# Performance work log

Hardware: AMD Instinct MI355X
Metric: run time of the kernel (lower is better)

Reference implementation:

```python
import jax, jax.numpy as jnp
import numpy as np

F_IN, D_MODEL, D_STATE, D_CONV, EXPAND = 20, 256, 64, 4, 2
D_INNER = EXPAND * D_MODEL  # 512
DT_RANK = D_MODEL // 16     # 16
BATCH, SEQ = 64, 1024


def setup_inputs() -> dict:
    key = jax.random.key(0)
    ks = jax.random.split(key, 12)
    s = lambda k, shape, sc: jax.random.normal(k, shape, dtype=jnp.float32) * sc
    inp = {
        "x": jax.random.normal(ks[0], (BATCH, SEQ, F_IN), dtype=jnp.float32),
        "embed_w": s(ks[1], (F_IN, D_MODEL), 0.1),
        "embed_b": jnp.zeros((D_MODEL,), jnp.float32),
        "in_proj_w": s(ks[2], (D_MODEL, 2 * D_INNER), 0.05),
        "conv_w": s(ks[3], (D_CONV, D_INNER), 0.2),
        "conv_b": jnp.zeros((D_INNER,), jnp.float32),
        "x_proj_w": s(ks[4], (D_INNER, DT_RANK + 2 * D_STATE), 0.05),
        "dt_proj_w": s(ks[5], (DT_RANK, D_INNER), 0.1),
        "dt_proj_b": jnp.full((D_INNER,), -4.6, jnp.float32),  # softplus ~ 0.01
        "A_log": jnp.log(jnp.tile(jnp.arange(1, D_STATE + 1, dtype=jnp.float32), (D_INNER, 1))),
        "D": jnp.ones((D_INNER,), jnp.float32),
        "out_proj_w": s(ks[6], (D_INNER, D_MODEL), 0.05),
        "ln_g": jnp.ones((D_MODEL,), jnp.float32),
        "ln_b": jnp.zeros((D_MODEL,), jnp.float32),
        "reg1_w": s(ks[7], (D_MODEL, 64), 0.1),
        "reg1_b": jnp.zeros((64,), jnp.float32),
        "reg2_w": s(ks[8], (64, 1), 0.1),
        "reg2_b": jnp.zeros((1,), jnp.float32),
    }
    return inp


def _forward(x, embed_w, embed_b, in_proj_w, conv_w, conv_b, x_proj_w,
             dt_proj_w, dt_proj_b, A_log, D, out_proj_w, ln_g, ln_b,
             reg1_w, reg1_b, reg2_w, reg2_b):
    h = x @ embed_w + embed_b                       # [B,L,Dm]
    residual = h
    xz = h @ in_proj_w                               # [B,L,2*Di]
    xi, z = jnp.split(xz, 2, axis=-1)                # each [B,L,Di]
    L = xi.shape[1]
    d_conv = conv_w.shape[0]
    # causal depthwise conv1d over time
    xp = jnp.pad(xi, ((0, 0), (d_conv - 1, 0), (0, 0)))
    conv = sum(xp[:, k:k + L, :] * conv_w[k] for k in range(d_conv)) + conv_b
    xc = jax.nn.silu(conv)                           # [B,L,Di]
    dbc = xc @ x_proj_w                              # [B,L,dt_rank+2N]
    dt_rank = dt_proj_w.shape[0]
    n = A_log.shape[1]
    dt, Bm, Cm = jnp.split(dbc, [dt_rank, dt_rank + n], axis=-1)
    delta = jax.nn.softplus(dt @ dt_proj_w + dt_proj_b)  # [B,L,Di]
    A = -jnp.exp(A_log)                              # [Di,N]

    def step(hst, t):
        delta_t, u_t, B_t, C_t = t                   # [B,Di],[B,Di],[B,N],[B,N]
        dA = jnp.exp(delta_t[..., None] * A)         # [B,Di,N]
        hst = hst * dA + (delta_t * u_t)[..., None] * B_t[:, None, :]
        y = jnp.einsum('bdn,bn->bd', hst, C_t)
        return hst, y

    bsz, d_inner = xc.shape[0], xc.shape[2]
    h0 = jnp.zeros((bsz, d_inner, n), xc.dtype)
    xs = (delta.transpose(1, 0, 2), xc.transpose(1, 0, 2),
          Bm.transpose(1, 0, 2), Cm.transpose(1, 0, 2))
    _, ys = jax.lax.scan(step, h0, xs)               # ys: [L,B,Di]
    y = ys.transpose(1, 0, 2) + xc * D               # skip term u*D
    y = y * jax.nn.silu(z)                           # gate
    out = y @ out_proj_w + residual                  # [B,L,Dm]
    mu = out.mean(-1, keepdims=True)
    var = out.var(-1, keepdims=True)
    out = (out - mu) / jnp.sqrt(var + 1e-5) * ln_g + ln_b
    feats = out[:, -1, :]                            # last timestep [B,Dm]
    hreg = jax.nn.relu(feats @ reg1_w + reg1_b)      # dropout inert at eval
    return (hreg @ reg2_w + reg2_b).squeeze(-1)      # [B]


def reference(x, embed_w, embed_b, in_proj_w, conv_w, conv_b, x_proj_w,
              dt_proj_w, dt_proj_b, A_log, D, out_proj_w, ln_g, ln_b,
              reg1_w, reg1_b, reg2_w, reg2_b):
    return _forward(x, embed_w, embed_b, in_proj_w, conv_w, conv_b, x_proj_w,
                    dt_proj_w, dt_proj_b, A_log, D, out_proj_w, ln_g, ln_b,
                    reg1_w, reg1_b, reg2_w, reg2_b)
```

## Files before the change

### kernel.cpp

```cpp
#include <hip/hip_runtime.h>
#include <math.h>

#define BATCH  64
#define SEQL   1024
#define FIN    20
#define DM     256
#define DIN    512
#define NST    64
#define RK     16
#define NTOK   (BATCH*SEQL)
#define NCHUNK 4
#define CLEN   (SEQL/NCHUNK)

typedef float v2f __attribute__((ext_vector_type(2)));

__device__ __forceinline__ float siluf(float v) { return v / (1.f + __expf(-v)); }

__global__ void k_wc(const float* __restrict__ We, const float* __restrict__ be,
                     const float* __restrict__ W1, float* __restrict__ Wc,
                     float* __restrict__ bc) {
    int j = threadIdx.x;
    int k = blockIdx.x;
    float acc = 0.f;
    if (k < FIN) {
        const float* wr = We + k*DM;
        for (int c = 0; c < DM; ++c) acc = fmaf(wr[c], W1[(size_t)c*1024 + j], acc);
        Wc[k*DIN + j] = acc;
    } else {
        for (int c = 0; c < DM; ++c) acc = fmaf(be[c], W1[(size_t)c*1024 + j], acc);
        bc[j] = acc;
    }
}

__global__ __launch_bounds__(512) void k_xiconv(const float* __restrict__ x,
        const float* __restrict__ Wc, const float* __restrict__ bc,
        const float* __restrict__ cw, const float* __restrict__ cb,
        float* __restrict__ xc) {
    const int TT = 16;
    __shared__ float xs[(TT+3)*FIN];
    __shared__ float xils[(TT+3)*DIN];
    int tid = threadIdx.x;
    int blk = blockIdx.x;
    int b   = blk >> 6;
    int seg = blk & 63;
    int t0  = seg * TT;

    for (int i = tid; i < (TT+3)*FIN; i += 512) {
        int tt = i / FIN;
        int kk = i - tt*FIN;
        int t  = t0 - 3 + tt;
        xs[i] = (t >= 0) ? x[((size_t)b*SEQL + t)*FIN + kk] : 0.f;
    }
    float w[FIN];
    #pragma unroll
    for (int k = 0; k < FIN; ++k) w[k] = Wc[k*DIN + tid];
    float bb = bc[tid];
    __syncthreads();

    for (int tt = 0; tt < TT+3; ++tt) {
        float acc = bb;
        #pragma unroll
        for (int k = 0; k < FIN; ++k) acc = fmaf(xs[tt*FIN + k], w[k], acc);
        int t = t0 - 3 + tt;
        xils[tt*DIN + tid] = (t >= 0) ? acc : 0.f;
    }
    float cwr[4];
    #pragma unroll
    for (int k = 0; k < 4; ++k) cwr[k] = cw[k*DIN + tid];
    float cbr = cb[tid];
    __syncthreads();

    for (int tt = 0; tt < TT; ++tt) {
        float a = cbr;
        #pragma unroll
        for (int k = 0; k < 4; ++k) a = fmaf(xils[(tt+k)*DIN + tid], cwr[k], a);
        a = siluf(a);
        xc[((size_t)b*SEQL + t0 + tt)*DIN + tid] = a;
    }
}

__global__ __launch_bounds__(256) void k_dtb(const float* __restrict__ xc,
        const float* __restrict__ xpw, float* __restrict__ dtB) {
    __shared__ float xs[64][65];
    int tid  = threadIdx.x;
    int tok0 = blockIdx.x * 64;
    int tok  = tid & 63;
    int og   = __builtin_amdgcn_readfirstlane(tid >> 6);
    float acc[20];
    #pragma unroll
    for (int j = 0; j < 20; ++j) acc[j] = 0.f;

    for (int kc = 0; kc < DIN; kc += 64) {
        __syncthreads();
        #pragma unroll
        for (int i = 0; i < 16; ++i) {
            int flat = i*256 + tid;
            int tk = flat >> 6, kk = flat & 63;
            xs[kk][tk] = xc[(size_t)(tok0+tk)*DIN + kc + kk];
        }
        __syncthreads();
        const float* wbase = xpw + (size_t)kc*144 + og*20;
        #pragma unroll 2
        for (int k = 0; k < 64; ++k) {
            float xv = xs[k][tok];
            const float* wr = wbase + (size_t)k*144;
            #pragma unroll
            for (int j = 0; j < 20; ++j)
                acc[j] = fmaf(xv, wr[j], acc[j]);
        }
    }
    float4* dst = (float4*)(dtB + (size_t)(tok0+tok)*80 + og*20);
    #pragma unroll
    for (int jq = 0; jq < 5; ++jq)
        dst[jq] = make_float4(acc[4*jq], acc[4*jq+1], acc[4*jq+2], acc[4*jq+3]);
}

__global__ __launch_bounds__(256) void k_scan(const float* __restrict__ xc,
        const float* __restrict__ dtB, const float* __restrict__ dpw,
        const float* __restrict__ dpb, float* __restrict__ cs,
        float* __restrict__ sdout) {
    const int W = 32;
    __shared__ __align__(16) float Bs[W][64];
    __shared__ __align__(16) float dl[W][128];
    int bid   = blockIdx.x;
    int b     = bid >> 4;
    int chunk = (bid >> 2) & 3;
    int dgB   = bid & 3;
    int tid   = threadIdx.x;
    int ns   = tid >> 5;
    int chg  = tid & 31;
    int d0   = dgB*128 + chg*4;
    float k1 = (float)(8*ns + 1);
    int srow = tid >> 3, scol = tid & 7;
    int dch = tid >> 1, kh = tid & 1;
    int ddc = dgB*128 + dch;

    float wd[8];
    #pragma unroll
    for (int k = 0; k < 8; ++k) wd[k] = dpw[(size_t)(8*kh+k)*DIN + ddc];
    float bias = dpb[ddc];
    float sdel = 0.f;

    v2f h2[4][4];
    #pragma unroll
    for (int dd = 0; dd < 4; ++dd)
        #pragma unroll
        for (int j = 0; j < 4; ++j) { h2[dd][j].x = 0.f; h2[dd][j].y = 0.f; }

    size_t tok0 = (size_t)b*SEQL + chunk*CLEN;
    float4 uv = *(const float4*)&xc[tok0*DIN + d0];

    #pragma unroll 1
    for (int w = 0; w < CLEN/W; ++w) {
        size_t wt0 = tok0 + (size_t)w*W;
        float4 s0 = *(const float4*)&dtB[(wt0+srow)*80 + 16 + scol*8];
        float4 s1 = *(const float4*)&dtB[(wt0+srow)*80 + 16 + scol*8 + 4];
        __syncthreads();
        *(float4*)&Bs[srow][scol*8]     = s0;
        *(float4*)&Bs[srow][scol*8 + 4] = s1;
        #pragma unroll 2
        for (int t = 0; t < W; ++t) {
            const float4* qp = (const float4*)&dtB[(wt0+t)*80 + kh*8];
            float4 q0 = qp[0], q1 = qp[1];
            float part = q0.x*wd[0];
            part = fmaf(q0.y, wd[1], part);
            part = fmaf(q0.z, wd[2], part);
            part = fmaf(q0.w, wd[3], part);
            part = fmaf(q1.x, wd[4], part);
            part = fmaf(q1.y, wd[5], part);
            part = fmaf(q1.z, wd[6], part);
            part = fmaf(q1.w, wd[7], part);
            part += __shfl_xor(part, 1, 64);
            float s  = part + bias;
            float dv = (s > 20.f) ? s : __logf(1.f + __expf(s));
            sdel += dv;
            if (kh == 0) dl[t][dch] = dv;
        }
        __syncthreads();
        #pragma unroll 2
        for (int tt = 0; tt < W; ++tt) {
            float4 uvn = *(const float4*)&xc[(wt0 + tt + 1)*DIN + d0];
            float4 dlv = *(const float4*)&dl[tt][chg*4];
            float4 ba  = *(const float4*)&Bs[tt][8*ns];
            float4 bb  = *(const float4*)&Bs[tt][8*ns + 4];
            v2f bv0, bv1, bv2, bv3;
            bv0.x = ba.x; bv0.y = ba.y;
            bv1.x = ba.z; bv1.y = ba.w;
            bv2.x = bb.x; bv2.y = bb.y;
            bv3.x = bb.z; bv3.y = bb.w;
            float dla[4] = {dlv.x, dlv.y, dlv.z, dlv.w};
            float uva[4] = {uv.x, uv.y, uv.z, uv.w};
            #pragma unroll
            for (int dd = 0; dd < 4; ++dd) {
                float dlc = dla[dd];
                float E   = __expf(-dlc);
                float p   = __expf(-dlc*k1);
                float c   = dlc * uva[dd];
                float E2  = E*E;
                v2f pv; pv.x = p;  pv.y = p*E;
                v2f e2; e2.x = E2; e2.y = E2;
                v2f cc; cc.x = c;  cc.y = c;
                h2[dd][0] = h2[dd][0]*pv + cc*bv0; pv *= e2;
                h2[dd][1] = h2[dd][1]*pv + cc*bv1; pv *= e2;
                h2[dd][2] = h2[dd][2]*pv + cc*bv2; pv *= e2;
                h2[dd][3] = h2[dd][3]*pv + cc*bv3;
            }
            uv = uvn;
        }
    }
    size_t base = ((size_t)(b*NCHUNK + chunk)*NST)*DIN;
    #pragma unroll
    for (int dd = 0; dd < 4; ++dd)
        #pragma unroll
        for (int j = 0; j < 4; ++j) {
            cs[base + (size_t)(8*ns + 2*j    )*DIN + d0 + dd] = h2[dd][j].x;
            cs[base + (size_t)(8*ns + 2*j + 1)*DIN + d0 + dd] = h2[dd][j].y;
        }
    if (kh == 0)
        sdout[(size_t)(b*NCHUNK + chunk)*DIN + ddc] = sdel;
}

__global__ __launch_bounds__(512) void k_tail(
        const float* __restrict__ x, const float* __restrict__ We,
        const float* __restrict__ be, const float* __restrict__ W1,
        const float* __restrict__ xc, const float* __restrict__ xpw,
        const float* __restrict__ cs, const float* __restrict__ sd,
        const float* __restrict__ Alog, const float* __restrict__ Dv,
        const float* __restrict__ Wout, const float* __restrict__ lng,
        const float* __restrict__ lnb, const float* __restrict__ r1w,
        const float* __restrict__ r1b, const float* __restrict__ r2w,
        const float* __restrict__ r2b, float* __restrict__ out) {
    __shared__ float xrow[FIN];
    __shared__ float hl[DM];
    __shared__ float xl[DIN];
    __shared__ float cls[NST];
    __shared__ float yl[DIN];
    __shared__ float os[DM];
    __shared__ float red[20];
    __shared__ float feats[DM];
    __shared__ float cpart[8][64];
    int b = blockIdx.x, tid = threadIdx.x;

    if (tid < FIN) xrow[tid] = x[((size_t)b*SEQL + SEQL-1)*FIN + tid];
    xl[tid] = xc[((size_t)b*SEQL + SEQL-1)*DIN + tid];
    __syncthreads();
    if (tid < DM) {
        float a = be[tid];
        #pragma unroll
        for (int k = 0; k < FIN; ++k) a = fmaf(xrow[k], We[k*DM + tid], a);
        hl[tid] = a;
    }
    __syncthreads();
    float z = 0.f;
    for (int c = 0; c < DM; ++c)
        z = fmaf(hl[c], W1[(size_t)c*1024 + DIN + tid], z);
    {
        int n = tid & 63, sl = tid >> 6;
        float a = 0.f;
        for (int kk = 0; kk < 64; ++kk)
            a = fmaf(xl[sl*64 + kk], xpw[(size_t)(sl*64 + kk)*144 + 80 + n], a);
        cpart[sl][n] = a;
    }
    __syncthreads();
    if (tid < 64) {
        float a = 0.f;
        #pragma unroll
        for (int i = 0; i < 8; ++i) a += cpart[i][tid];
        cls[tid] = a;
    }
    __syncthreads();
    float s1 = sd[((size_t)b*NCHUNK + 1)*DIN + tid];
    float s2 = sd[((size_t)b*NCHUNK + 2)*DIN + tid];
    float s3 = sd[((size_t)b*NCHUNK + 3)*DIN + tid];
    const size_t CSTR = (size_t)NST*DIN;
    size_t cb = ((size_t)b*NCHUNK)*CSTR + tid;
    float y = 0.f;
    #pragma unroll 8
    for (int n = 0; n < NST; ++n) {
        float A  = -__expf(Alog[(size_t)tid*NST + n]);
        float hh = cs[cb + (size_t)n*DIN];
        hh = fmaf(hh, __expf(A*s1), cs[cb + CSTR   + (size_t)n*DIN]);
        hh = fmaf(hh, __expf(A*s2), cs[cb + 2*CSTR + (size_t)n*DIN]);
        hh = fmaf(hh, __expf(A*s3), cs[cb + 3*CSTR + (size_t)n*DIN]);
        y  = fmaf(hh, cls[n], y);
    }
    float yv = y + xl[tid]*Dv[tid];
    yl[tid]  = yv * siluf(z);
    __syncthreads();
    {
        int o = tid >> 1, hf = tid & 1;
        float a = 0.f;
        for (int dd = hf*256; dd < hf*256 + 256; ++dd)
            a = fmaf(yl[dd], Wout[(size_t)dd*DM + o], a);
        a += __shfl_xor(a, 1, 64);
        if (hf == 0) os[o] = a + hl[o];
    }
    __syncthreads();
    float accv = (tid < DM) ? os[tid] : 0.f;
    float t1 = accv, t2 = accv*accv;
    #pragma unroll
    for (int o = 32; o > 0; o >>= 1) {
        t1 += __shfl_down(t1, o, 64);
        t2 += __shfl_down(t2, o, 64);
    }
    if (tid < DM && (tid & 63) == 0) { red[tid>>6] = t1; red[8+(tid>>6)] = t2; }
    __syncthreads();
    if (tid == 0) {
        float a1 = 0.f, a2 = 0.f;
        for (int w = 0; w < 4; ++w) { a1 += red[w]; a2 += red[8+w]; }
        red[16] = a1; red[17] = a2;
    }
    __syncthreads();
    if (tid < DM) {
        float mu   = red[16]*(1.f/DM);
        float var  = red[17]*(1.f/DM) - mu*mu;
        float rstd = rsqrtf(var + 1e-5f);
        feats[tid] = (accv - mu)*rstd*lng[tid] + lnb[tid];
    }
    __syncthreads();
    if (tid < 64) {
        float r = r1b[tid];
        for (int i = 0; i < DM; ++i) r = fmaf(feats[i], r1w[(size_t)i*64 + tid], r);
        r = fmaxf(r, 0.f);
        float v = r * r2w[tid];
        #pragma unroll
        for (int o = 32; o > 0; o >>= 1) v += __shfl_down(v, o, 64);
        if (tid == 0) out[b] = v + r2b[0];
    }
}

extern "C" void kernel_launch(void* const* d_in, const int* in_sizes, int n_in,
                              void* d_out, int out_size, void* d_ws, size_t ws_size,
                              hipStream_t stream) {
    (void)in_sizes; (void)n_in; (void)out_size; (void)ws_size;
    const float* x    = (const float*)d_in[0];
    const float* We   = (const float*)d_in[1];
    const float* be   = (const float*)d_in[2];
    const float* W1   = (const float*)d_in[3];
    const float* cw   = (const float*)d_in[4];
    const float* cb   = (const float*)d_in[5];
    const float* xpw  = (const float*)d_in[6];
    const float* dpw  = (const float*)d_in[7];
    const float* dpb  = (const float*)d_in[8];
    const float* Alog = (const float*)d_in[9];
    const float* Dv   = (const float*)d_in[10];
    const float* Wout = (const float*)d_in[11];
    const float* lng  = (const float*)d_in[12];
    const float* lnb  = (const float*)d_in[13];
    const float* r1w  = (const float*)d_in[14];
    const float* r1b  = (const float*)d_in[15];
    const float* r2w  = (const float*)d_in[16];
    const float* r2b  = (const float*)d_in[17];
    float* out = (float*)d_out;

    float* ws = (float*)d_ws;
    size_t off = 0;
    float* xc  = ws + off; off += (size_t)(NTOK+1)*DIN;
    float* dtB = ws + off; off += (size_t)NTOK*80;
    float* Wc  = ws + off; off += (size_t)FIN*DIN;
    float* bc  = ws + off; off += DIN;
    float* cs  = ws + off; off += (size_t)BATCH*NCHUNK*NST*DIN;
    float* sd  = ws + off; off += (size_t)BATCH*NCHUNK*DIN;

    k_wc     <<<FIN+1,    DIN, 0, stream>>>(We, be, W1, Wc, bc);
    k_xiconv <<<NTOK/16,  512, 0, stream>>>(x, Wc, bc, cw, cb, xc);
    k_dtb    <<<NTOK/64,  256, 0, stream>>>(xc, xpw, dtB);
    k_scan   <<<BATCH*NCHUNK*4, 256, 0, stream>>>(xc, dtB, dpw, dpb, cs, sd);
    k_tail   <<<BATCH,    512, 0, stream>>>(x, We, be, W1, xc, xpw, cs, sd,
                                            Alog, Dv, Wout, lng, lnb,
                                            r1w, r1b, r2w, r2b, out);
}
```

Measured before the change: 422.0 us.

## Remap scan threads to 2 channels x 16 states and precompute exp decay

```diff
diff --git a/kernel.cpp b/kernel.cpp
--- a/kernel.cpp
+++ b/kernel.cpp
@@ -13,6 +13,7 @@
 #define CLEN   (SEQL/NCHUNK)
 
 typedef float v2f __attribute__((ext_vector_type(2)));
+typedef float v4f __attribute__((ext_vector_type(4)));
 
 __device__ __forceinline__ float siluf(float v) { return v / (1.f + __expf(-v)); }
 
@@ -115,25 +116,51 @@
         dst[jq] = make_float4(acc[4*jq], acc[4*jq+1], acc[4*jq+2], acc[4*jq+3]);
 }
 
+#define CH_UPDATE(HR, DLT, EV, UU)                                        \
+    do {                                                                  \
+        float c_  = (DLT) * (UU);                                         \
+        float E_  = (EV);                                                 \
+        float E2_ = E_*E_;                                                \
+        float E4_ = E2_*E2_;                                              \
+        float E8_ = E4_*E4_;                                              \
+        float E16_= E8_*E8_;                                              \
+        float E32_= E16_*E16_;                                            \
+        float m_  = ((ns & 1) ? E16_ : 1.f) * ((ns & 2) ? E32_ : 1.f);    \
+        float p0_ = m_ * E_;                                              \
+        v2f pv_; pv_.x = p0_; pv_.y = p0_*E_;                             \
+        v2f e2_; e2_.x = E2_; e2_.y = E2_;                                \
+        v2f cc_; cc_.x = c_;  cc_.y = c_;                                 \
+        HR[0] = HR[0]*pv_ + cc_*bv0; pv_ *= e2_;                          \
+        HR[1] = HR[1]*pv_ + cc_*bv1; pv_ *= e2_;                          \
+        HR[2] = HR[2]*pv_ + cc_*bv2; pv_ *= e2_;                          \
+        HR[3] = HR[3]*pv_ + cc_*bv3; pv_ *= e2_;                          \
+        HR[4] = HR[4]*pv_ + cc_*bv4; pv_ *= e2_;                          \
+        HR[5] = HR[5]*pv_ + cc_*bv5; pv_ *= e2_;                          \
+        HR[6] = HR[6]*pv_ + cc_*bv6; pv_ *= e2_;                          \
+        HR[7] = HR[7]*pv_ + cc_*bv7;                                      \
+    } while (0)
+
 __global__ __launch_bounds__(256) void k_scan(const float* __restrict__ xc,
         const float* __restrict__ dtB, const float* __restrict__ dpw,
         const float* __restrict__ dpb, float* __restrict__ cs,
         float* __restrict__ sdout) {
     const int W = 32;
-    __shared__ __align__(16) float Bs[W][64];
-    __shared__ __align__(16) float dl[W][128];
+    __shared__ __align__(16) float  Bs[W][64];
+    __shared__ __align__(16) float2 dEs[W][128];
     int bid   = blockIdx.x;
     int b     = bid >> 4;
     int chunk = (bid >> 2) & 3;
     int dgB   = bid & 3;
     int tid   = threadIdx.x;
-    int ns   = tid >> 5;
-    int chg  = tid & 31;
-    int d0   = dgB*128 + chg*4;
-    float k1 = (float)(8*ns + 1);
-    int srow = tid >> 3, scol = tid & 7;
+    int w     = tid >> 6;
+    int lane  = tid & 63;
+    int ns    = lane >> 4;
+    int chg   = lane & 15;
+    int chL   = w*32 + chg*2;
+    int d0    = dgB*128 + chL;
     int dch = tid >> 1, kh = tid & 1;
     int ddc = dgB*128 + dch;
+    int srow = tid >> 4, scol = tid & 15;
 
     float wd[8];
     #pragma unroll
@@ -141,23 +168,23 @@
     float bias = dpb[ddc];
     float sdel = 0.f;
 
-    v2f h2[4][4];
-    #pragma unroll
-    for (int dd = 0; dd < 4; ++dd)
-        #pragma unroll
-        for (int j = 0; j < 4; ++j) { h2[dd][j].x = 0.f; h2[dd][j].y = 0.f; }
+    v2f h2a[8], h2b[8];
+    #pragma unroll
+    for (int j = 0; j < 8; ++j) {
+        h2a[j].x = 0.f; h2a[j].y = 0.f;
+        h2b[j].x = 0.f; h2b[j].y = 0.f;
+    }
 
     size_t tok0 = (size_t)b*SEQL + chunk*CLEN;
-    float4 uv = *(const float4*)&xc[tok0*DIN + d0];
 
     #pragma unroll 1
-    for (int w = 0; w < CLEN/W; ++w) {
-        size_t wt0 = tok0 + (size_t)w*W;
-        float4 s0 = *(const float4*)&dtB[(wt0+srow)*80 + 16 + scol*8];
-        float4 s1 = *(const float4*)&dtB[(wt0+srow)*80 + 16 + scol*8 + 4];
+    for (int wn = 0; wn < CLEN/W; ++wn) {
+        size_t wt0 = tok0 + (size_t)wn*W;
+        float4 sB0 = *(const float4*)&dtB[(wt0+srow)*80    + 16 + scol*4];
+        float4 sB1 = *(const float4*)&dtB[(wt0+16+srow)*80 + 16 + scol*4];
         __syncthreads();
-        *(float4*)&Bs[srow][scol*8]     = s0;
-        *(float4*)&Bs[srow][scol*8 + 4] = s1;
+        *(float4*)&Bs[srow][scol*4]      = sB0;
+        *(float4*)&Bs[16+srow][scol*4]   = sB1;
         #pragma unroll 2
         for (int t = 0; t < W; ++t) {
             const float4* qp = (const float4*)&dtB[(wt0+t)*80 + kh*8];
@@ -174,48 +201,35 @@
             float s  = part + bias;
             float dv = (s > 20.f) ? s : __logf(1.f + __expf(s));
             sdel += dv;
-            if (kh == 0) dl[t][dch] = dv;
+            float Ev = __expf(-dv);
+            if (kh == 0) dEs[t][dch] = make_float2(dv, Ev);
         }
         __syncthreads();
         #pragma unroll 2
         for (int tt = 0; tt < W; ++tt) {
-            float4 uvn = *(const float4*)&xc[(wt0 + tt + 1)*DIN + d0];
-            float4 dlv = *(const float4*)&dl[tt][chg*4];
-            float4 ba  = *(const float4*)&Bs[tt][8*ns];
-            float4 bb  = *(const float4*)&Bs[tt][8*ns + 4];
-            v2f bv0, bv1, bv2, bv3;
-            bv0.x = ba.x; bv0.y = ba.y;
-            bv1.x = ba.z; bv1.y = ba.w;
-            bv2.x = bb.x; bv2.y = bb.y;
-            bv3.x = bb.z; bv3.y = bb.w;
-            float dla[4] = {dlv.x, dlv.y, dlv.z, dlv.w};
-            float uva[4] = {uv.x, uv.y, uv.z, uv.w};
-            #pragma unroll
-            for (int dd = 0; dd < 4; ++dd) {
-                float dlc = dla[dd];
-                float E   = __expf(-dlc);
-                float p   = __expf(-dlc*k1);
-                float c   = dlc * uva[dd];
-                float E2  = E*E;
-                v2f pv; pv.x = p;  pv.y = p*E;
-                v2f e2; e2.x = E2; e2.y = E2;
-                v2f cc; cc.x = c;  cc.y = c;
-                h2[dd][0] = h2[dd][0]*pv + cc*bv0; pv *= e2;
-                h2[dd][1] = h2[dd][1]*pv + cc*bv1; pv *= e2;
-                h2[dd][2] = h2[dd][2]*pv + cc*bv2; pv *= e2;
-                h2[dd][3] = h2[dd][3]*pv + cc*bv3;
-            }
-            uv = uvn;
+            float4 de4 = *(const float4*)&dEs[tt][chL];
+            float2 u2  = *(const float2*)&xc[(wt0+tt)*DIN + d0];
+            const v4f* Bp = (const v4f*)&Bs[tt][16*ns];
+            v4f B0 = Bp[0], B1 = Bp[1], B2 = Bp[2], B3 = Bp[3];
+            v2f bv0 = __builtin_shufflevector(B0, B0, 0, 1);
+            v2f bv1 = __builtin_shufflevector(B0, B0, 2, 3);
+            v2f bv2 = __builtin_shufflevector(B1, B1, 0, 1);
+            v2f bv3 = __builtin_shufflevector(B1, B1, 2, 3);
+            v2f bv4 = __builtin_shufflevector(B2, B2, 0, 1);
+            v2f bv5 = __builtin_shufflevector(B2, B2, 2, 3);
+            v2f bv6 = __builtin_shufflevector(B3, B3, 0, 1);
+            v2f bv7 = __builtin_shufflevector(B3, B3, 2, 3);
+            CH_UPDATE(h2a, de4.x, de4.y, u2.x);
+            CH_UPDATE(h2b, de4.z, de4.w, u2.y);
         }
     }
     size_t base = ((size_t)(b*NCHUNK + chunk)*NST)*DIN;
     #pragma unroll
-    for (int dd = 0; dd < 4; ++dd)
-        #pragma unroll
-        for (int j = 0; j < 4; ++j) {
-            cs[base + (size_t)(8*ns + 2*j    )*DIN + d0 + dd] = h2[dd][j].x;
-            cs[base + (size_t)(8*ns + 2*j + 1)*DIN + d0 + dd] = h2[dd][j].y;
-        }
+    for (int j = 0; j < 8; ++j) {
+        int n0 = 16*ns + 2*j;
+        *(float2*)&cs[base + (size_t)n0*DIN     + d0] = make_float2(h2a[j].x, h2b[j].x);
+        *(float2*)&cs[base + (size_t)(n0+1)*DIN + d0] = make_float2(h2a[j].y, h2b[j].y);
+    }
     if (kh == 0)
         sdout[(size_t)(b*NCHUNK + chunk)*DIN + ddc] = sdel;
 }
```

Result: slower. 432.7 us (+2.5%).
